# Optimization experiments

Hardware: AMD Instinct MI355X
Metric: run time of the kernel (lower is better)

Reference implementation:

```python
import jax, jax.numpy as jnp
import numpy as np

N_SRC = 100000
N_TGT = 100000
N_EDGES = 1600000
D = 128
HID = 128
OUT = 64
NUM_LAYERS = 2
P_DROP = 0.1
NEG_SLOPE = 0.01


def setup_inputs() -> dict:
    key = jax.random.key(0)
    ks = jax.random.split(key, 16)
    s = 1.0 / np.sqrt(D)
    inp = {
        "x_source": jax.random.normal(ks[0], (N_SRC, D), jnp.float32),
        "x_target": jax.random.normal(ks[1], (N_TGT, D), jnp.float32),
        "Wl_tgt": jax.random.normal(ks[2], (NUM_LAYERS, D, HID), jnp.float32) * s,
        "bl_tgt": jax.random.normal(ks[3], (NUM_LAYERS, HID), jnp.float32) * s,
        "Wr_tgt": jax.random.normal(ks[4], (NUM_LAYERS, D, HID), jnp.float32) * s,
        "Wl_src": jax.random.normal(ks[5], (NUM_LAYERS, D, HID), jnp.float32) * s,
        "bl_src": jax.random.normal(ks[6], (NUM_LAYERS, HID), jnp.float32) * s,
        "Wr_src": jax.random.normal(ks[7], (NUM_LAYERS, D, HID), jnp.float32) * s,
        "W_out": jax.random.normal(ks[8], (HID, OUT), jnp.float32) * (1.0 / np.sqrt(HID)),
        "b_out": jax.random.normal(ks[9], (OUT,), jnp.float32) * 0.01,
        "edge_src": jax.random.randint(ks[10], (N_EDGES,), 0, N_SRC, jnp.int32),
        "edge_dst": jax.random.randint(ks[11], (N_EDGES,), 0, N_TGT, jnp.int32),
        "rev_src": jax.random.randint(ks[12], (N_EDGES,), 0, N_TGT, jnp.int32),
        "rev_dst": jax.random.randint(ks[13], (N_EDGES,), 0, N_SRC, jnp.int32),
    }
    return inp


def _sage(x_src, x_dst, src_idx, dst_idx, n_dst, Wl, bl, Wr):
    # mean-aggregate neighbor messages per destination node (PyG SAGEConv default)
    msg = x_src[src_idx]  # [E, D] gather
    agg = jax.ops.segment_sum(msg, dst_idx, num_segments=n_dst)  # [n_dst, D]
    cnt = jax.ops.segment_sum(jnp.ones((src_idx.shape[0],), msg.dtype), dst_idx,
                              num_segments=n_dst)
    mean = agg / jnp.maximum(cnt, 1.0)[:, None]
    return mean @ Wl + bl + x_dst @ Wr


def _dropout(x, key):
    keep = jax.random.bernoulli(key, 1.0 - P_DROP, x.shape)
    return jnp.where(keep, x / (1.0 - P_DROP), jnp.zeros((), x.dtype))


def reference(x_source, x_target, Wl_tgt, bl_tgt, Wr_tgt, Wl_src, bl_src, Wr_src,
              W_out, b_out, edge_src, edge_dst, rev_src, rev_dst):
    dkey = jax.random.key(42)
    xs, xt = x_source, x_target
    for l in range(NUM_LAYERS):
        # ('source','edge','target'): target receives from source
        new_t = _sage(xs, xt, edge_src, edge_dst, N_TGT, Wl_tgt[l], bl_tgt[l], Wr_tgt[l])
        # ('target','rev_edge','source'): source receives from target
        new_s = _sage(xt, xs, rev_src, rev_dst, N_SRC, Wl_src[l], bl_src[l], Wr_src[l])
        new_t = jax.nn.leaky_relu(new_t, NEG_SLOPE)
        new_s = jax.nn.leaky_relu(new_s, NEG_SLOPE)
        new_t = _dropout(new_t, jax.random.fold_in(dkey, 2 * l))
        new_s = _dropout(new_s, jax.random.fold_in(dkey, 2 * l + 1))
        xs, xt = new_s, new_t
    return xs @ W_out + b_out
```

## Files before the change

kernel.cpp:

```cpp
#include <hip/hip_runtime.h>
#include <stdint.h>

#define NN 100000
#define NE 1600000
#define DD 128
#define PS 48
#define HB 1024
#define G8 12544
#define SUBN 98
#define NSUB 128
#define NND 100352
#define K2 16
#define RCAP 2304

typedef unsigned short u16;
typedef short short8 __attribute__((ext_vector_type(8)));
typedef float floatx4 __attribute__((ext_vector_type(4)));
typedef int intx4 __attribute__((ext_vector_type(4)));

__device__ static inline u16 f2bf(float f){
  unsigned u = __float_as_uint(f);
  unsigned r = u + 0x7FFFu + ((u >> 16) & 1u);
  return (u16)(r >> 16);
}

__host__ __device__ static inline unsigned rotl32(unsigned x, int r){
  return (x << r) | (x >> (32 - r));
}

__host__ __device__ static inline void tf2x32(unsigned k0, unsigned k1,
                                              unsigned c0, unsigned c1,
                                              unsigned &o0, unsigned &o1)
{
  const unsigned ks2 = k0 ^ k1 ^ 0x1BD11BDAu;
  unsigned x0 = c0 + k0, x1 = c1 + k1;
#define TFR(r) { x0 += x1; x1 = rotl32(x1, (r)); x1 ^= x0; }
  TFR(13) TFR(15) TFR(26) TFR(6)   x0 += k1;  x1 += ks2 + 1u;
  TFR(17) TFR(29) TFR(16) TFR(24)  x0 += ks2; x1 += k0 + 2u;
  TFR(13) TFR(15) TFR(26) TFR(6)   x0 += k0;  x1 += k1 + 3u;
  TFR(17) TFR(29) TFR(16) TFR(24)  x0 += k1;  x1 += ks2 + 4u;
  TFR(13) TFR(15) TFR(26) TFR(6)   x0 += ks2; x1 += k0 + 5u;
#undef TFR
  o0 = x0; o1 = x1;
}

__device__ static inline float drop_scale(unsigned k0, unsigned k1, unsigned j)
{
  unsigned o0, o1;
  tf2x32(k0, k1, 0u, j, o0, o1);
  const unsigned bits = o0 ^ o1;
  const float u = __uint_as_float((bits >> 9) | 0x3F800000u) - 1.0f;
  return (u < 0.9f) ? (1.0f / 0.9f) : 0.0f;
}

__global__ __launch_bounds__(256) void k_hist(const int* __restrict__ e_dst,
                                              const int* __restrict__ r_dst,
                                              int* __restrict__ hist){
  __shared__ int h[16];
  const int t = threadIdx.x;
  if (t < 16) h[t] = 0;
  __syncthreads();
  const int QT = 2 * (NE / 4);
  for (int i = blockIdx.x * 256 + t; i < QT; i += HB * 256){
    int dir = (i >= NE / 4);
    int qi = dir ? i - NE / 4 : i;
    const int* dp = dir ? r_dst : e_dst;
    intx4 d = __builtin_nontemporal_load((const intx4*)dp + qi);
    int bb = dir << 3;
    atomicAdd(&h[bb + d.x / G8], 1);
    atomicAdd(&h[bb + d.y / G8], 1);
    atomicAdd(&h[bb + d.z / G8], 1);
    atomicAdd(&h[bb + d.w / G8], 1);
  }
  __syncthreads();
  if (t < 16) hist[t * HB + blockIdx.x] = h[t];
}

__global__ __launch_bounds__(256) void k_scanA(int* __restrict__ hist){
  __shared__ int sh[16 * HB];
  __shared__ int tot[256];
  const int t = threadIdx.x;
  const int N = 16 * HB;
  for (int k = t; k < N; k += 256) sh[k] = hist[k];
  __syncthreads();
  int s = 0;
  #pragma unroll 4
  for (int k = 0; k < 64; ++k)
    s += sh[(t >> 4) * HB + (t & 15) + (k << 4)];
  tot[t] = s;
  __syncthreads();
  int v = s;
  for (int off = 1; off < 256; off <<= 1){
    int u = (t >= off) ? tot[t - off] : 0;
    __syncthreads();
    tot[t] += u;
    __syncthreads();
  }
  int run = tot[t] - v;
  for (int k = 0; k < 64; ++k){
    int idx = (t >> 4) * HB + (t & 15) + (k << 4);
    int xv = sh[idx];
    sh[idx] = run;
    run += xv;
  }
  __syncthreads();
  for (int k = t; k < N; k += 256) hist[k] = sh[k];
  if (t == 255) hist[N] = tot[255];
}

__global__ __launch_bounds__(256) void k_scatter1(const int* __restrict__ e_src,
                                                  const int* __restrict__ e_dst,
                                                  const int* __restrict__ r_src,
                                                  const int* __restrict__ r_dst,
                                                  const int* __restrict__ base,
                                                  unsigned* __restrict__ stage){
  __shared__ int cur[16];
  const int t = threadIdx.x;
  if (t < 16) cur[t] = base[t * HB + blockIdx.x];
  __syncthreads();
  const int QT = 2 * (NE / 4);
  for (int i = blockIdx.x * 256 + t; i < QT; i += HB * 256){
    int dir = (i >= NE / 4);
    int qi = dir ? i - NE / 4 : i;
    const int* dp = dir ? r_dst : e_dst;
    const int* sp = dir ? r_src : e_src;
    intx4 d = __builtin_nontemporal_load((const intx4*)dp + qi);
    intx4 sv = __builtin_nontemporal_load((const intx4*)sp + qi);
    int bb = dir << 3;
    int g, p;
    g = d.x / G8; p = atomicAdd(&cur[bb + g], 1);
    stage[p] = (unsigned)sv.x | ((unsigned)(d.x - g * G8) << 17);
    g = d.y / G8; p = atomicAdd(&cur[bb + g], 1);
    stage[p] = (unsigned)sv.y | ((unsigned)(d.y - g * G8) << 17);
    g = d.z / G8; p = atomicAdd(&cur[bb + g], 1);
    stage[p] = (unsigned)sv.z | ((unsigned)(d.z - g * G8) << 17);
    g = d.w / G8; p = atomicAdd(&cur[bb + g], 1);
    stage[p] = (unsigned)sv.w | ((unsigned)(d.w - g * G8) << 17);
  }
}

__global__ __launch_bounds__(256) void k_hist2(const unsigned* __restrict__ stage,
                                               const int* __restrict__ base,
                                               int* __restrict__ hist2){
  __shared__ int h2[NSUB];
  const int b16 = blockIdx.x / K2, k = blockIdx.x % K2;
  const int t = threadIdx.x;
  if (t < NSUB) h2[t] = 0;
  __syncthreads();
  const int beg = base[b16 * HB];
  const int end = base[(b16 + 1) * HB];
  for (int i = beg + k * 256 + t; i < end; i += K2 * 256){
    unsigned p = stage[i];
    atomicAdd(&h2[(int)(p >> 17) / SUBN], 1);
  }
  __syncthreads();
  if (t < NSUB) hist2[(b16 * NSUB + t) * K2 + k] = h2[t];
}

__global__ __launch_bounds__(256) void k_scanB(int* __restrict__ hist2){
  __shared__ int sh[16 * NSUB * K2];
  __shared__ int tot[256];
  const int t = threadIdx.x;
  const int N = 16 * NSUB * K2;
  for (int k = t; k < N; k += 256) sh[k] = hist2[k];
  __syncthreads();
  int s = 0;
  for (int j = 0; j < 128; ++j) s += sh[t * 128 + j];
  tot[t] = s;
  __syncthreads();
  int v = s;
  for (int off = 1; off < 256; off <<= 1){
    int u = (t >= off) ? tot[t - off] : 0;
    __syncthreads();
    tot[t] += u;
    __syncthreads();
  }
  int run = tot[t] - v;
  for (int j = 0; j < 128; ++j){
    int xv = sh[t * 128 + j];
    sh[t * 128 + j] = run;
    run += xv;
  }
  __syncthreads();
  for (int k = t; k < N; k += 256) hist2[k] = sh[k];
}

__global__ __launch_bounds__(256) void k_scatter2(const unsigned* __restrict__ stage,
                                                  const int* __restrict__ base,
                                                  const int* __restrict__ h2s,
                                                  unsigned* __restrict__ stage2){
  __shared__ int cur[NSUB];
  const int b16 = blockIdx.x / K2, k = blockIdx.x % K2;
  const int t = threadIdx.x;
  if (t < NSUB) cur[t] = h2s[(b16 * NSUB + t) * K2 + k];
  __syncthreads();
  const int beg = base[b16 * HB];
  const int end = base[(b16 + 1) * HB];
  for (int i = beg + k * 256 + t; i < end; i += K2 * 256){
    unsigned p = stage[i];
    int pos = atomicAdd(&cur[(int)(p >> 17) / SUBN], 1);
    stage2[pos] = p;
  }
}

__global__ __launch_bounds__(256) void k_fill3(const unsigned* __restrict__ stage2,
                                               const int* __restrict__ h2s,
                                               int* __restrict__ deg,
                                               int* __restrict__ csr){
  __shared__ unsigned rec[RCAP];
  __shared__ unsigned srt[RCAP];
  __shared__ int ldeg[SUBN], lptr[SUBN], lcur[SUBN];
  const int sb = blockIdx.x;
  const int b16 = sb >> 7, sub = sb & 127;
  const int dir = b16 >> 3, g = b16 & 7;
  const int t = threadIdx.x;
  const int beg = h2s[sb * K2];
  const int end = (sb == 2047) ? 2 * NE : h2s[(sb + 1) * K2];
  int n = end - beg;
  if (n > RCAP) n = RCAP;
  for (int i = t; i < n; i += 256) rec[i] = stage2[beg + i];
  if (t < SUBN) ldeg[t] = 0;
  __syncthreads();
  const int nl0 = sub * SUBN;
  for (int i = t; i < n; i += 256)
    atomicAdd(&ldeg[(int)(rec[i] >> 17) - nl0], 1);
  __syncthreads();
  if (t == 0){
    int run = 0;
    for (int s = 0; s < SUBN; ++s){ lptr[s] = run; lcur[s] = run; run += ldeg[s]; }
  }
  __syncthreads();
  for (int i = t; i < n; i += 256){
    int rl = (int)(rec[i] >> 17) - nl0;
    int pos = atomicAdd(&lcur[rl], 1);
    srt[pos] = rec[i] & 0x1FFFFu;
  }
  __syncthreads();
  const int node0 = g * G8 + nl0;
  int* degd = deg + dir * NND;
  int* csrd = csr + (size_t)dir * NND * PS;
  if (t < SUBN) degd[node0 + t] = ldeg[t];
  const int base4 = node0 * (PS / 4);
  for (int j4 = t; j4 < SUBN * (PS / 4); j4 += 256){
    int row = j4 / (PS / 4);
    int s4 = (j4 % (PS / 4)) * 4;
    int d0 = ldeg[row], p0 = lptr[row];
    uint4 v;
    v.x = (s4 + 0 < d0) ? srt[p0 + s4 + 0] : 0u;
    v.y = (s4 + 1 < d0) ? srt[p0 + s4 + 1] : 0u;
    v.z = (s4 + 2 < d0) ? srt[p0 + s4 + 2] : 0u;
    v.w = (s4 + 3 < d0) ? srt[p0 + s4 + 3] : 0u;
    ((uint4*)csrd)[base4 + j4] = v;
  }
}

__global__ __launch_bounds__(256) void k_cvt2(const float* __restrict__ ina,
                                              const float* __restrict__ inb,
                                              u16* __restrict__ oa,
                                              u16* __restrict__ ob, int n8){
  int i = blockIdx.x * 256 + threadIdx.x;
  const float* in = ina; u16* out = oa;
  if (i >= n8){ i -= n8; in = inb; out = ob; }
  floatx4 a = __builtin_nontemporal_load((const floatx4*)in + (size_t)i * 2);
  floatx4 b = __builtin_nontemporal_load((const floatx4*)in + (size_t)i * 2 + 1);
  u16 v[8] = { f2bf(a[0]), f2bf(a[1]), f2bf(a[2]), f2bf(a[3]),
               f2bf(b[0]), f2bf(b[1]), f2bf(b[2]), f2bf(b[3]) };
  *(uint4*)(out + (size_t)i * 8) = *(const uint4*)v;
}

__global__ __launch_bounds__(256) void k_prep(const float* __restrict__ Wl_tgt,
    const float* __restrict__ Wr_tgt, const float* __restrict__ Wl_src,
    const float* __restrict__ Wr_src, const float* __restrict__ Wo,
    u16* __restrict__ Wsw0, u16* __restrict__ Wsw1, u16* __restrict__ Wsw2,
    u16* __restrict__ Wswo){
  int b = blockIdx.x;
  if (b < 48){
    const float *Wl, *Wr; u16* dst;
    if (b < 16){ Wl = Wl_tgt; Wr = Wr_tgt; dst = Wsw0; }
    else if (b < 32){ Wl = Wl_src; Wr = Wr_src; dst = Wsw1; b -= 16; }
    else { Wl = Wl_src + 16384; Wr = Wr_src + 16384; dst = Wsw2; b -= 32; }
    int idx = b * 256 + threadIdx.x;
    int lane = idx & 63, tile = idx >> 6;
    int kt = tile >> 3, nt = tile & 7;
    int n = nt * 16 + (lane & 15);
    int kb = kt * 32 + (lane >> 4) * 8;
    u16 v[8];
    #pragma unroll
    for (int j = 0; j < 8; ++j){
      int k = kb + j;
      float w = (k < 128) ? Wl[(size_t)k * 128 + n] : Wr[(size_t)(k - 128) * 128 + n];
      v[j] = f2bf(w);
    }
    *(uint4*)(dst + (size_t)idx * 8) = *(const uint4*)v;
  } else {
    int idx = (b - 48) * 256 + threadIdx.x;
    int lane = idx & 63, tile = idx >> 6;
    int kt = tile >> 2, nt = tile & 3;
    int n = nt * 16 + (lane & 15);
    int kb = kt * 32 + (lane >> 4) * 8;
    u16 v[8];
    #pragma unroll
    for (int j = 0; j < 8; ++j)
      v[j] = f2bf(Wo[(size_t)(kb + j) * 64 + n]);
    *(uint4*)(Wswo + (size_t)idx * 8) = *(const uint4*)v;
  }
}

__global__ __launch_bounds__(256) void k_agg(const u16* __restrict__ x,
                                             const int* __restrict__ deg,
                                             const int* __restrict__ csr,
                                             u16* __restrict__ out){
  const int row  = blockIdx.x * 4 + (threadIdx.x >> 6);
  const int lane = threadIdx.x & 63;
  const int sub = lane >> 4, l4 = lane & 15;
  int cnt = deg[row];
  if (cnt > PS) cnt = PS;
  const int beg = row * PS;
  float a[8] = {0.f,0.f,0.f,0.f,0.f,0.f,0.f,0.f};
  int e = 0;
  for (; e + 7 < cnt; e += 8){
    int s0 = csr[beg + e + sub];
    int s1 = csr[beg + e + 4 + sub];
    uint4 v0 = *(const uint4*)(x + (size_t)s0 * DD + l4 * 8);
    uint4 v1 = *(const uint4*)(x + (size_t)s1 * DD + l4 * 8);
    a[0] += __uint_as_float(v0.x << 16); a[1] += __uint_as_float(v0.x & 0xFFFF0000u);
    a[2] += __uint_as_float(v0.y << 16); a[3] += __uint_as_float(v0.y & 0xFFFF0000u);
    a[4] += __uint_as_float(v0.z << 16); a[5] += __uint_as_float(v0.z & 0xFFFF0000u);
    a[6] += __uint_as_float(v0.w << 16); a[7] += __uint_as_float(v0.w & 0xFFFF0000u);
    a[0] += __uint_as_float(v1.x << 16); a[1] += __uint_as_float(v1.x & 0xFFFF0000u);
    a[2] += __uint_as_float(v1.y << 16); a[3] += __uint_as_float(v1.y & 0xFFFF0000u);
    a[4] += __uint_as_float(v1.z << 16); a[5] += __uint_as_float(v1.z & 0xFFFF0000u);
    a[6] += __uint_as_float(v1.w << 16); a[7] += __uint_as_float(v1.w & 0xFFFF0000u);
  }
  for (; e + 3 < cnt; e += 4){
    int s0 = csr[beg + e + sub];
    uint4 v0 = *(const uint4*)(x + (size_t)s0 * DD + l4 * 8);
    a[0] += __uint_as_float(v0.x << 16); a[1] += __uint_as_float(v0.x & 0xFFFF0000u);
    a[2] += __uint_as_float(v0.y << 16); a[3] += __uint_as_float(v0.y & 0xFFFF0000u);
    a[4] += __uint_as_float(v0.z << 16); a[5] += __uint_as_float(v0.z & 0xFFFF0000u);
    a[6] += __uint_as_float(v0.w << 16); a[7] += __uint_as_float(v0.w & 0xFFFF0000u);
  }
  if (e + sub < cnt){
    int s0 = csr[beg + e + sub];
    uint4 v0 = *(const uint4*)(x + (size_t)s0 * DD + l4 * 8);
    a[0] += __uint_as_float(v0.x << 16); a[1] += __uint_as_float(v0.x & 0xFFFF0000u);
    a[2] += __uint_as_float(v0.y << 16); a[3] += __uint_as_float(v0.y & 0xFFFF0000u);
    a[4] += __uint_as_float(v0.z << 16); a[5] += __uint_as_float(v0.z & 0xFFFF0000u);
    a[6] += __uint_as_float(v0.w << 16); a[7] += __uint_as_float(v0.w & 0xFFFF0000u);
  }
  #pragma unroll
  for (int i = 0; i < 8; ++i){
    a[i] += __shfl_xor(a[i], 16);
    a[i] += __shfl_xor(a[i], 32);
  }
  const float inv = (cnt > 0) ? (1.0f / (float)cnt) : 1.0f;
  if (sub == 0){
    unsigned pk[4];
    #pragma unroll
    for (int i = 0; i < 4; ++i)
      pk[i] = (unsigned)f2bf(a[2*i] * inv) | ((unsigned)f2bf(a[2*i+1] * inv) << 16);
    *(uint4*)(out + (size_t)row * DD + l4 * 8) = make_uint4(pk[0], pk[1], pk[2], pk[3]);
  }
}

__global__ __launch_bounds__(256) void k_fused(const u16* __restrict__ Am,
    const u16* __restrict__ X, const u16* __restrict__ Wsw,
    const float* __restrict__ bias, u16* __restrict__ outH,
    unsigned key0, unsigned key1)
{
  const int wave = threadIdx.x >> 6, lane = threadIdx.x & 63;
  const int quad = lane >> 4, col0 = lane & 15;
  const int row0 = blockIdx.x * 64 + wave * 16;
  int m = row0 + col0;
  if (m >= NN) m = NN - 1;

  floatx4 acc[8];
  #pragma unroll
  for (int i = 0; i < 8; ++i) acc[i] = (floatx4)0.f;

  #pragma unroll
  for (int kt = 0; kt < 8; ++kt){
    const int k = kt * 32 + quad * 8;
    const u16* ap = (k < 128) ? (Am + (size_t)m * 128 + k)
                              : (X  + (size_t)m * 128 + (k - 128));
    short8 a = __builtin_nontemporal_load((const short8*)ap);
    #pragma unroll
    for (int nt = 0; nt < 8; ++nt){
      short8 b = *(const short8*)(Wsw + (size_t)(((kt * 8 + nt) * 64 + lane) * 8));
      acc[nt] = __builtin_amdgcn_mfma_f32_16x16x32_bf16(a, b, acc[nt], 0, 0, 0);
    }
  }

  #pragma unroll
  for (int nt = 0; nt < 8; ++nt){
    const int col = nt * 16 + col0;
    const float bj = bias[col];
    #pragma unroll
    for (int rg = 0; rg < 4; ++rg){
      const int r = row0 + quad * 4 + rg;
      if (r < NN){
        float h = acc[nt][rg] + bj;
        h = (h >= 0.f) ? h : 0.01f * h;
        unsigned j = (unsigned)r * 128u + (unsigned)col;
        h *= drop_scale(key0, key1, j);
        outH[(size_t)r * 128 + col] = f2bf(h);
      }
    }
  }
}

__global__ __launch_bounds__(256) void k_out(const u16* __restrict__ H,
    const u16* __restrict__ Wsw, const float* __restrict__ bias,
    float* __restrict__ out)
{
  const int wave = threadIdx.x >> 6, lane = threadIdx.x & 63;
  const int quad = lane >> 4, col0 = lane & 15;
  const int row0 = blockIdx.x * 64 + wave * 16;
  int m = row0 + col0;
  if (m >= NN) m = NN - 1;

  floatx4 acc[4];
  #pragma unroll
  for (int i = 0; i < 4; ++i) acc[i] = (floatx4)0.f;

  #pragma unroll
  for (int kt = 0; kt < 4; ++kt){
    short8 a = __builtin_nontemporal_load(
        (const short8*)(H + (size_t)m * 128 + kt * 32 + quad * 8));
    #pragma unroll
    for (int nt = 0; nt < 4; ++nt){
      short8 b = *(const short8*)(Wsw + (size_t)(((kt * 4 + nt) * 64 + lane) * 8));
      acc[nt] = __builtin_amdgcn_mfma_f32_16x16x32_bf16(a, b, acc[nt], 0, 0, 0);
    }
  }

  #pragma unroll
  for (int nt = 0; nt < 4; ++nt){
    const int col = nt * 16 + col0;
    const float bj = bias[col];
    #pragma unroll
    for (int rg = 0; rg < 4; ++rg){
      const int r = row0 + quad * 4 + rg;
      if (r < NN)
        out[(size_t)r * 64 + col] = acc[nt][rg] + bj;
    }
  }
}

extern "C" void kernel_launch(void* const* d_in, const int* in_sizes, int n_in,
                              void* d_out, int out_size, void* d_ws, size_t ws_size,
                              hipStream_t stream)
{
  const float* x_src  = (const float*)d_in[0];
  const float* x_tgt  = (const float*)d_in[1];
  const float* Wl_tgt = (const float*)d_in[2];
  const float* bl_tgt = (const float*)d_in[3];
  const float* Wr_tgt = (const float*)d_in[4];
  const float* Wl_src = (const float*)d_in[5];
  const float* bl_src = (const float*)d_in[6];
  const float* Wr_src = (const float*)d_in[7];
  const float* W_o    = (const float*)d_in[8];
  const float* b_o    = (const float*)d_in[9];
  const int*   e_src  = (const int*)d_in[10];
  const int*   e_dst  = (const int*)d_in[11];
  const int*   r_src  = (const int*)d_in[12];
  const int*   r_dst  = (const int*)d_in[13];
  float* out = (float*)d_out;
  (void)in_sizes; (void)n_in; (void)out_size; (void)ws_size;

  char* ws = (char*)d_ws;
  size_t off = 0;
  auto alloc = [&](size_t bytes) -> char* {
    char* p = ws + off; off += (bytes + 255) & ~(size_t)255; return p;
  };
  unsigned* stage1 = (unsigned*)alloc((size_t)2 * NE * 4);
  unsigned* stage2 = (unsigned*)alloc((size_t)2 * NE * 4);
  u16* A     = (u16*)stage1;
  u16* Xs    = (u16*)alloc((size_t)NN * DD * 2);
  u16* Xt    = (u16*)alloc((size_t)NN * DD * 2);
  u16* B     = (u16*)alloc((size_t)NN * DD * 2);
  u16* C     = (u16*)alloc((size_t)NN * DD * 2);
  u16* Wsw0  = (u16*)alloc(256 * 128 * 2);
  u16* Wsw1  = (u16*)alloc(256 * 128 * 2);
  u16* Wsw2  = (u16*)alloc(256 * 128 * 2);
  u16* Wswo  = (u16*)alloc(128 * 64 * 2);
  int* deg   = (int*)alloc((size_t)2 * NND * 4);
  int* csr   = (int*)alloc((size_t)2 * NND * PS * 4);
  int* hist  = (int*)alloc((size_t)(16 * HB + 1) * 4);
  int* hist2 = (int*)alloc((size_t)(16 * NSUB * K2) * 4);

  unsigned kt0a, kt0b, ks0a, ks0b, ks1a, ks1b;
  tf2x32(0u, 42u, 0u, 0u, kt0a, kt0b);
  tf2x32(0u, 42u, 0u, 1u, ks0a, ks0b);
  tf2x32(0u, 42u, 0u, 3u, ks1a, ks1b);

  const int CB = NN * DD / 8 / 256;

  k_cvt2<<<2 * CB, 256, 0, stream>>>(x_src, x_tgt, Xs, Xt, NN * DD / 8);
  k_prep<<<52, 256, 0, stream>>>(Wl_tgt, Wr_tgt, Wl_src, Wr_src, W_o,
                                 Wsw0, Wsw1, Wsw2, Wswo);

  k_hist<<<HB, 256, 0, stream>>>(e_dst, r_dst, hist);
  k_scanA<<<1, 256, 0, stream>>>(hist);
  k_scatter1<<<HB, 256, 0, stream>>>(e_src, e_dst, r_src, r_dst, hist, stage1);
  k_hist2<<<16 * K2, 256, 0, stream>>>(stage1, hist, hist2);
  k_scanB<<<1, 256, 0, stream>>>(hist2);
  k_scatter2<<<16 * K2, 256, 0, stream>>>(stage1, hist, hist2, stage2);
  k_fill3<<<2048, 256, 0, stream>>>(stage2, hist2, deg, csr);

  const int GB = (NN + 63) / 64;
  const int AB = NN / 4;
  const int*   deg_t = deg;
  const int*   deg_s = deg + NND;
  const int*   csr_e = csr;
  const int*   csr_r = csr + (size_t)NND * PS;
  k_agg<<<AB, 256, 0, stream>>>(Xs, deg_t, csr_e, A);
  k_fused<<<GB, 256, 0, stream>>>(A, Xt, Wsw0, bl_tgt, B, kt0a, kt0b);
  k_agg<<<AB, 256, 0, stream>>>(Xt, deg_s, csr_r, A);
  k_fused<<<GB, 256, 0, stream>>>(A, Xs, Wsw1, bl_src, C, ks0a, ks0b);
  k_agg<<<AB, 256, 0, stream>>>(B, deg_s, csr_r, A);
  k_fused<<<GB, 256, 0, stream>>>(A, C, Wsw2, bl_src + 128, B, ks1a, ks1b);
  k_out<<<GB, 256, 0, stream>>>(B, Wswo, b_o, out);
}
```

Baseline: 589.9 us.

## Switch padded CSR to compact CSR and merge both layer-0 directions into one launch

Replaces the fixed-width padded neighbor table (48 slots per node, truncating higher degrees) with a compact CSR array plus row pointers, written straight from the sorted shared-memory buffer. The layer-0 aggregation and fused GEMM kernels for both edge directions are merged into single launches that split work by block index. This cuts the bytes the fill kernel writes and the launch count, and fills the GPU better in layer 0. It costs an extra aggregation buffer and pointer loads per row, and it also stops dropping neighbors beyond 48.

```diff
diff --git a/kernel.cpp b/kernel.cpp
--- a/kernel.cpp
+++ b/kernel.cpp
@@ -4,7 +4,6 @@
 #define NN 100000
 #define NE 1600000
 #define DD 128
-#define PS 48
 #define HB 1024
 #define G8 12544
 #define SUBN 98
@@ -203,9 +202,9 @@
   }
 }
 
-__global__ __launch_bounds__(256) void k_fill3(const unsigned* __restrict__ stage2,
+__global__ __launch_bounds__(256) void k_fill4(const unsigned* __restrict__ stage2,
                                                const int* __restrict__ h2s,
-                                               int* __restrict__ deg,
+                                               int* __restrict__ ptr,
                                                int* __restrict__ csr){
   __shared__ unsigned rec[RCAP];
   __shared__ unsigned srt[RCAP];
@@ -237,21 +236,9 @@
   }
   __syncthreads();
   const int node0 = g * G8 + nl0;
-  int* degd = deg + dir * NND;
-  int* csrd = csr + (size_t)dir * NND * PS;
-  if (t < SUBN) degd[node0 + t] = ldeg[t];
-  const int base4 = node0 * (PS / 4);
-  for (int j4 = t; j4 < SUBN * (PS / 4); j4 += 256){
-    int row = j4 / (PS / 4);
-    int s4 = (j4 % (PS / 4)) * 4;
-    int d0 = ldeg[row], p0 = lptr[row];
-    uint4 v;
-    v.x = (s4 + 0 < d0) ? srt[p0 + s4 + 0] : 0u;
-    v.y = (s4 + 1 < d0) ? srt[p0 + s4 + 1] : 0u;
-    v.z = (s4 + 2 < d0) ? srt[p0 + s4 + 2] : 0u;
-    v.w = (s4 + 3 < d0) ? srt[p0 + s4 + 3] : 0u;
-    ((uint4*)csrd)[base4 + j4] = v;
-  }
+  if (t < SUBN) ptr[dir * NND + node0 + t] = beg + lptr[t];
+  if (sb == 2047 && t == 0) ptr[2 * NND] = 2 * NE;
+  for (int i = t; i < n; i += 256) csr[beg + i] = (int)srt[i];
 }
 
 __global__ __launch_bounds__(256) void k_cvt2(const float* __restrict__ ina,
@@ -306,16 +293,15 @@
   }
 }
 
-__global__ __launch_bounds__(256) void k_agg(const u16* __restrict__ x,
-                                             const int* __restrict__ deg,
-                                             const int* __restrict__ csr,
-                                             u16* __restrict__ out){
-  const int row  = blockIdx.x * 4 + (threadIdx.x >> 6);
+__device__ static inline void agg_body(const u16* __restrict__ x,
+                                       const int* __restrict__ pd,
+                                       const int* __restrict__ csr,
+                                       u16* __restrict__ out, int blk){
+  const int row = blk * 4 + (threadIdx.x >> 6);
   const int lane = threadIdx.x & 63;
   const int sub = lane >> 4, l4 = lane & 15;
-  int cnt = deg[row];
-  if (cnt > PS) cnt = PS;
-  const int beg = row * PS;
+  const int beg = pd[row], end = pd[row + 1];
+  const int cnt = end - beg;
   float a[8] = {0.f,0.f,0.f,0.f,0.f,0.f,0.f,0.f};
   int e = 0;
   for (; e + 7 < cnt; e += 8){
@@ -363,14 +349,28 @@
   }
 }
 
-__global__ __launch_bounds__(256) void k_fused(const u16* __restrict__ Am,
+__global__ __launch_bounds__(256) void k_aggD(const u16* __restrict__ x0,
+    const u16* __restrict__ x1, const int* __restrict__ ptr,
+    const int* __restrict__ csr, u16* __restrict__ o0, u16* __restrict__ o1){
+  int b = blockIdx.x;
+  if (b < NN / 4) agg_body(x0, ptr, csr, o0, b);
+  else            agg_body(x1, ptr + NND, csr, o1, b - NN / 4);
+}
+
+__global__ __launch_bounds__(256) void k_agg1(const u16* __restrict__ x,
+    const int* __restrict__ ptr, const int* __restrict__ csr,
+    u16* __restrict__ out){
+  agg_body(x, ptr + NND, csr, out, blockIdx.x);
+}
+
+__device__ static inline void fused_body(const u16* __restrict__ Am,
     const u16* __restrict__ X, const u16* __restrict__ Wsw,
     const float* __restrict__ bias, u16* __restrict__ outH,
-    unsigned key0, unsigned key1)
+    unsigned key0, unsigned key1, int blk)
 {
   const int wave = threadIdx.x >> 6, lane = threadIdx.x & 63;
   const int quad = lane >> 4, col0 = lane & 15;
-  const int row0 = blockIdx.x * 64 + wave * 16;
+  const int row0 = blk * 64 + wave * 16;
   int m = row0 + col0;
   if (m >= NN) m = NN - 1;
 
@@ -407,6 +407,29 @@
       }
     }
   }
+}
+
+#define GB ((NN + 63) / 64)
+
+__global__ __launch_bounds__(256) void k_fusedD(
+    const u16* __restrict__ A0, const u16* __restrict__ X0,
+    const u16* __restrict__ W0, const float* __restrict__ b0,
+    u16* __restrict__ o0, unsigned k00, unsigned k01,
+    const u16* __restrict__ A1, const u16* __restrict__ X1,
+    const u16* __restrict__ W1, const float* __restrict__ b1,
+    u16* __restrict__ o1, unsigned k10, unsigned k11)
+{
+  int b = blockIdx.x;
+  if (b < GB) fused_body(A0, X0, W0, b0, o0, k00, k01, b);
+  else        fused_body(A1, X1, W1, b1, o1, k10, k11, b - GB);
+}
+
+__global__ __launch_bounds__(256) void k_fused(const u16* __restrict__ Am,
+    const u16* __restrict__ X, const u16* __restrict__ Wsw,
+    const float* __restrict__ bias, u16* __restrict__ outH,
+    unsigned key0, unsigned key1)
+{
+  fused_body(Am, X, Wsw, bias, outH, key0, key1, blockIdx.x);
 }
 
 __global__ __launch_bounds__(256) void k_out(const u16* __restrict__ H,
@@ -475,17 +498,18 @@
   };
   unsigned* stage1 = (unsigned*)alloc((size_t)2 * NE * 4);
   unsigned* stage2 = (unsigned*)alloc((size_t)2 * NE * 4);
-  u16* A     = (u16*)stage1;
-  u16* Xs    = (u16*)alloc((size_t)NN * DD * 2);
-  u16* Xt    = (u16*)alloc((size_t)NN * DD * 2);
-  u16* B     = (u16*)alloc((size_t)NN * DD * 2);
-  u16* C     = (u16*)alloc((size_t)NN * DD * 2);
-  u16* Wsw0  = (u16*)alloc(256 * 128 * 2);
-  u16* Wsw1  = (u16*)alloc(256 * 128 * 2);
-  u16* Wsw2  = (u16*)alloc(256 * 128 * 2);
-  u16* Wswo  = (u16*)alloc(128 * 64 * 2);
-  int* deg   = (int*)alloc((size_t)2 * NND * 4);
-  int* csr   = (int*)alloc((size_t)2 * NND * PS * 4);
+  u16* A_t  = (u16*)stage1;
+  u16* A_s  = (u16*)alloc((size_t)NN * DD * 2);
+  u16* Xs   = (u16*)alloc((size_t)NN * DD * 2);
+  u16* Xt   = (u16*)alloc((size_t)NN * DD * 2);
+  u16* B    = (u16*)alloc((size_t)NN * DD * 2);
+  u16* C    = (u16*)alloc((size_t)NN * DD * 2);
+  u16* Wsw0 = (u16*)alloc(256 * 128 * 2);
+  u16* Wsw1 = (u16*)alloc(256 * 128 * 2);
+  u16* Wsw2 = (u16*)alloc(256 * 128 * 2);
+  u16* Wswo = (u16*)alloc(128 * 64 * 2);
+  int* csr  = (int*)alloc((size_t)2 * NE * 4);
+  int* ptr  = (int*)alloc((size_t)(2 * NND + 1) * 4);
   int* hist  = (int*)alloc((size_t)(16 * HB + 1) * 4);
   int* hist2 = (int*)alloc((size_t)(16 * NSUB * K2) * 4);
 
@@ -506,19 +530,13 @@
   k_hist2<<<16 * K2, 256, 0, stream>>>(stage1, hist, hist2);
   k_scanB<<<1, 256, 0, stream>>>(hist2);
   k_scatter2<<<16 * K2, 256, 0, stream>>>(stage1, hist, hist2, stage2);
-  k_fill3<<<2048, 256, 0, stream>>>(stage2, hist2, deg, csr);
-
-  const int GB = (NN + 63) / 64;
+  k_fill4<<<2048, 256, 0, stream>>>(stage2, hist2, ptr, csr);
+
   const int AB = NN / 4;
-  const int*   deg_t = deg;
-  const int*   deg_s = deg + NND;
-  const int*   csr_e = csr;
-  const int*   csr_r = csr + (size_t)NND * PS;
-  k_agg<<<AB, 256, 0, stream>>>(Xs, deg_t, csr_e, A);
-  k_fused<<<GB, 256, 0, stream>>>(A, Xt, Wsw0, bl_tgt, B, kt0a, kt0b);
-  k_agg<<<AB, 256, 0, stream>>>(Xt, deg_s, csr_r, A);
-  k_fused<<<GB, 256, 0, stream>>>(A, Xs, Wsw1, bl_src, C, ks0a, ks0b);
-  k_agg<<<AB, 256, 0, stream>>>(B, deg_s, csr_r, A);
-  k_fused<<<GB, 256, 0, stream>>>(A, C, Wsw2, bl_src + 128, B, ks1a, ks1b);
+  k_aggD<<<2 * AB, 256, 0, stream>>>(Xs, Xt, ptr, csr, A_t, A_s);
+  k_fusedD<<<2 * GB, 256, 0, stream>>>(A_t, Xt, Wsw0, bl_tgt, B, kt0a, kt0b,
+                                       A_s, Xs, Wsw1, bl_src, C, ks0a, ks0b);
+  k_agg1<<<AB, 256, 0, stream>>>(B, ptr, csr, A_t);
+  k_fused<<<GB, 256, 0, stream>>>(A_t, C, Wsw2, bl_src + 128, B, ks1a, ks1b);
   k_out<<<GB, 256, 0, stream>>>(B, Wswo, b_o, out);
 }
```

Result: no change. 578.8 us (-1.9%).
